# Kernel optimization log

Hardware: AMD Instinct MI355X
Metric: run time of the kernel (lower is better)

## Reference

```python
import jax, jax.numpy as jnp
import numpy as np

N_A = 50000
N_B = 50000
E = 500000
HID = 128
NEG_SLOPE = 0.2
LN_EPS = 1e-5


def _ln(x, g, b):
    mu = jnp.mean(x, axis=-1, keepdims=True)
    var = jnp.mean((x - mu) ** 2, axis=-1, keepdims=True)
    return (x - mu) * jax.lax.rsqrt(var + LN_EPS) * g + b


def _gat(x_src, x_dst, src, dst, W, a_src, a_dst, bias, H, D, n_dst):
    # PyG GATConv (shared lin for src/dst, add_self_loops=False, eval mode)
    hs = (x_src @ W).reshape(-1, H, D)              # [N_src, H, D]
    hd = (x_dst @ W).reshape(-1, H, D)              # [N_dst, H, D]
    a_s = jnp.einsum('nhd,hd->nh', hs, a_src)       # per-node src score
    a_d = jnp.einsum('nhd,hd->nh', hd, a_dst)       # per-node dst score
    e = jax.nn.leaky_relu(a_s[src] + a_d[dst], NEG_SLOPE)   # [E, H]
    m = jax.ops.segment_max(e, dst, num_segments=n_dst)     # segment softmax
    m = jnp.where(jnp.isfinite(m), m, 0.0)
    ex = jnp.exp(e - m[dst])
    s = jax.ops.segment_sum(ex, dst, num_segments=n_dst)
    alpha = ex / (s[dst] + 1e-16)                   # [E, H]
    msg = hs[src] * alpha[:, :, None]               # [E, H, D]
    out = jax.ops.segment_sum(msg, dst, num_segments=n_dst) # [N_dst, H, D]
    return out.reshape(n_dst, H * D) + bias


def setup_inputs() -> dict:
    key = jax.random.key(0)
    ks = jax.random.split(key, 32)
    f32 = jnp.float32

    def rn(k, sh, s=0.05):
        return jax.random.normal(k, sh, dtype=f32) * s

    inp = {}
    inp['x_A'] = jax.random.normal(ks[0], (N_A, 128), dtype=f32)
    inp['x_B'] = jax.random.normal(ks[1], (N_B, 64), dtype=f32)
    inp['pWA'] = rn(ks[2], (128, HID)); inp['pbA'] = rn(ks[3], (HID,))
    inp['pWB'] = rn(ks[4], (64, HID)); inp['pbB'] = rn(ks[5], (HID,))
    inp['w0ab'] = rn(ks[6], (HID, HID)); inp['as0ab'] = rn(ks[7], (4, 32))
    inp['ad0ab'] = rn(ks[8], (4, 32)); inp['b0ab'] = rn(ks[9], (HID,))
    inp['w0ba'] = rn(ks[10], (HID, HID)); inp['as0ba'] = rn(ks[11], (4, 32))
    inp['ad0ba'] = rn(ks[12], (4, 32)); inp['b0ba'] = rn(ks[13], (HID,))
    inp['w1ab'] = rn(ks[14], (HID, HID)); inp['as1ab'] = rn(ks[15], (1, HID))
    inp['ad1ab'] = rn(ks[16], (1, HID)); inp['b1ab'] = rn(ks[17], (HID,))
    inp['w1ba'] = rn(ks[18], (HID, HID)); inp['as1ba'] = rn(ks[19], (1, HID))
    inp['ad1ba'] = rn(ks[20], (1, HID)); inp['b1ba'] = rn(ks[21], (HID,))
    for i, nm in enumerate(['0A', '0B', '1A', '1B']):
        inp['g' + nm] = jnp.ones((HID,), dtype=f32)
        inp['bn' + nm] = jnp.zeros((HID,), dtype=f32)
    inp['ei_AB'] = jax.random.randint(ks[22], (2, E), 0, N_B)  # src in A, dst in B
    inp['ei_BA'] = jax.random.randint(ks[23], (2, E), 0, N_A)  # src in B, dst in A
    return inp


def reference(x_A, x_B, pWA, pbA, pWB, pbB,
              w0ab, as0ab, ad0ab, b0ab, w0ba, as0ba, ad0ba, b0ba,
              w1ab, as1ab, ad1ab, b1ab, w1ba, as1ba, ad1ba, b1ba,
              g0A, bn0A, g0B, bn0B, g1A, bn1A, g1B, bn1B,
              ei_AB, ei_BA):
    # input projections (dropout is eval-mode no-op)
    hA = x_A @ pWA + pbA
    hB = x_B @ pWB + pbB
    # layer 0: heads=4, d_head=32, concat -> 128
    pA, pB = hA, hB
    nB = _gat(hA, hB, ei_AB[0], ei_AB[1], w0ab, as0ab, ad0ab, b0ab, 4, 32, N_B)
    nA = _gat(hB, hA, ei_BA[0], ei_BA[1], w0ba, as0ba, ad0ba, b0ba, 4, 32, N_A)
    hA = jax.nn.relu(_ln(nA, g0A, bn0A)) + pA
    hB = jax.nn.relu(_ln(nB, g0B, bn0B)) + pB
    # layer 1: heads=1, out=128
    pA, pB = hA, hB
    nB = _gat(hA, hB, ei_AB[0], ei_AB[1], w1ab, as1ab, ad1ab, b1ab, 1, HID, N_B)
    nA = _gat(hB, hA, ei_BA[0], ei_BA[1], w1ba, as1ba, ad1ba, b1ba, 1, HID, N_A)
    hA = jax.nn.relu(_ln(nA, g1A, bn1A)) + pA
    hB = jax.nn.relu(_ln(nB, g1B, bn1B)) + pB
    return hA, hB
```

## Files before the change

### kernel.cpp

```cpp
#include <hip/hip_runtime.h>
#include <hip/hip_bf16.h>

using bf16 = __hip_bfloat16;
using frag8 = __attribute__((ext_vector_type(8))) short;
using f32x4 = __attribute__((ext_vector_type(4))) float;

__device__ __forceinline__ short f2bf_bits(float f) {
  bf16 h = __float2bfloat16(f);
  short s; __builtin_memcpy(&s, &h, 2); return s;
}
__device__ __forceinline__ float bfbits2f(unsigned short u) {
  unsigned uu = (unsigned)u << 16; float f; __builtin_memcpy(&f, &uu, 4); return f;
}
__device__ __forceinline__ float wred_sum(float v) {
#pragma unroll
  for (int o = 32; o; o >>= 1) v += __shfl_xor(v, o);
  return v;
}

struct ConvJob { const void* src; void* dst; int n; int mode; int ksh; };
struct ConvJobs { ConvJob j[28]; };
struct WtJob { const void* wraw; const void* adraw; bf16* out; int H; };
struct WtJobs4 { WtJob j[4]; };

__global__ __launch_bounds__(256) void prep_k(
    const unsigned* __restrict__ xdet, int* __restrict__ flag,
    ConvJobs cjobs, int ncv, WtJobs4 wjobs,
    int* __restrict__ cntA, int nA, int* __restrict__ cntB, int nB)
{
  const int b = blockIdx.x, tid = threadIdx.x;
  if (b >= ncv + 4) {
    int i = (b - (ncv + 4)) * 256 + tid;
    if (i < nA) cntA[i] = 0;
    else if (i < nA + nB) cntB[i - nA] = 0;
    return;
  }
  __shared__ int sh[256];
  int c = 0;
  for (int i = tid; i < 4096; i += 256) {
    unsigned bb = (xdet[i] >> 8) & 0x7F;
    c += (bb >= 0x3B && bb <= 0x41) ? 1 : 0;
  }
  sh[tid] = c; __syncthreads();
  for (int off = 128; off; off >>= 1) { if (tid < off) sh[tid] += sh[tid + off]; __syncthreads(); }
  const int f = (sh[0] < 2048) ? 1 : 0;
  if (b == 0 && tid == 0) flag[0] = f;

  if (b < ncv) {
    ConvJob J = cjobs.j[b];
    const int Kt = 1 << J.ksh;
    for (int i = tid; i < J.n; i += 256) {
      int si = i;
      if (J.mode == 1) { int n = i >> J.ksh, k = i & (Kt - 1); si = k * 128 + n; }
      float v = f ? ((const float*)J.src)[si] : bfbits2f(((const unsigned short*)J.src)[si]);
      if (J.mode == 1) ((bf16*)J.dst)[i] = __float2bfloat16(v);
      else             ((float*)J.dst)[i] = v;
    }
  } else {
    WtJob J = wjobs.j[b - ncv];
    const int H = J.H, D = 128 / H;
    for (int idx = tid; idx < 16 * 128; idx += 256) {
      int h = idx >> 7, k = idx & 127;
      float s = 0.f;
      if (h < H) {
        for (int d = 0; d < D; d++) {
          int n = h * D + d;
          float wv = f ? ((const float*)J.wraw)[k * 128 + n]
                       : bfbits2f(((const unsigned short*)J.wraw)[k * 128 + n]);
          float av = f ? ((const float*)J.adraw)[n]
                       : bfbits2f(((const unsigned short*)J.adraw)[n]);
          s += wv * av;
        }
      }
      J.out[idx] = __float2bfloat16(s);
    }
  }
}

struct GemmJob {
  const void* Av; const bf16* WT; const float* bias; const float* avec;
  bf16* outFull; float* outScore; const int* flagp;
  const bf16* WT2; float* outScore2;
  int M, K, H, H2;
};
__device__ __forceinline__ void gemm_body(const GemmJob& J, int blk) {
  __shared__ __align__(16) bf16 Wt[128 * 136];
  __shared__ __align__(16) bf16 Wt2s[16 * 136];
  const int tid = threadIdx.x;
  const int K = J.K;
  const int isf32 = J.flagp ? J.flagp[0] : 0;
  const int stride = K + 8;
  const int ksh2 = (K == 128) ? 4 : 3;
  const int kunits = K >> 3;
  for (int u = tid; u < 128 * kunits; u += 256) {
    int n = u >> ksh2, kb = u & (kunits - 1);
    frag8 v = *(const frag8*)(J.WT + n * K + kb * 8);
    *(frag8*)(Wt + n * stride + kb * 8) = v;
  }
  if (J.WT2) {
    int n = tid >> 4, kb = tid & 15;
    *(frag8*)(Wt2s + n * 136 + kb * 8) = *(const frag8*)(J.WT2 + n * 128 + kb * 8);
  }
  __syncthreads();

  const int lane = tid & 63, wave = tid >> 6;
  const int quad = lane >> 4, c = lane & 15;
  const int mbase = blk * 64 + wave * 16;
  const int arow = mbase + c;
  const bool rowOK = arow < J.M;

  f32x4 acc[8];
#pragma unroll
  for (int t = 0; t < 8; t++) acc[t] = (f32x4){0.f, 0.f, 0.f, 0.f};
  f32x4 acc2 = (f32x4){0.f, 0.f, 0.f, 0.f};

  for (int ks = 0; ks < K; ks += 32) {
    frag8 af;
    const int k0 = ks + quad * 8;
    if (rowOK) {
      if (isf32) {
        const float4* ap = (const float4*)((const float*)J.Av + (size_t)arow * K + k0);
        float4 v0 = ap[0], v1 = ap[1];
        af[0] = f2bf_bits(v0.x); af[1] = f2bf_bits(v0.y);
        af[2] = f2bf_bits(v0.z); af[3] = f2bf_bits(v0.w);
        af[4] = f2bf_bits(v1.x); af[5] = f2bf_bits(v1.y);
        af[6] = f2bf_bits(v1.z); af[7] = f2bf_bits(v1.w);
      } else {
        af = *(const frag8*)((const bf16*)J.Av + (size_t)arow * K + k0);
      }
    } else {
#pragma unroll
      for (int j = 0; j < 8; j++) af[j] = 0;
    }
#pragma unroll
    for (int t = 0; t < 8; t++) {
      frag8 bfv = *(const frag8*)(Wt + (t * 16 + c) * stride + k0);
      acc[t] = __builtin_amdgcn_mfma_f32_16x16x32_bf16(af, bfv, acc[t], 0, 0, 0);
    }
    if (J.WT2) {
      frag8 b2 = *(const frag8*)(Wt2s + c * 136 + k0);
      acc2 = __builtin_amdgcn_mfma_f32_16x16x32_bf16(af, b2, acc2, 0, 0, 0);
    }
  }

  if (J.outFull) {
#pragma unroll
    for (int t = 0; t < 8; t++) {
#pragma unroll
      for (int r = 0; r < 4; r++) {
        int orow = mbase + quad * 4 + r;
        if (orow < J.M) {
          float v = acc[t][r];
          if (J.bias) v += J.bias[t * 16 + c];
          J.outFull[(size_t)orow * 128 + t * 16 + c] = __float2bfloat16(v);
        }
      }
    }
  }
  if (J.outScore) {
    const int H = J.H;
    const int TPH = 8 / H;
    for (int hh = 0; hh < H; hh++) {
#pragma unroll
      for (int r = 0; r < 4; r++) {
        float p = 0.f;
        for (int tt = 0; tt < TPH; tt++) {
          int t = hh * TPH + tt;
          p += acc[t][r] * J.avec[t * 16 + c];
        }
#pragma unroll
        for (int off = 1; off < 16; off <<= 1) p += __shfl_xor(p, off);
        int orow = mbase + quad * 4 + r;
        if (c == 0 && orow < J.M) J.outScore[(size_t)orow * H + hh] = p;
      }
    }
  }
  if (J.outScore2) {
#pragma unroll
    for (int r = 0; r < 4; r++) {
      int orow = mbase + quad * 4 + r;
      if (c < J.H2 && orow < J.M) J.outScore2[(size_t)orow * J.H2 + c] = acc2[r];
    }
  }
}

__global__ __launch_bounds__(256) void histgemm_k(
    GemmJob ja, GemmJob jb, int gsplit,
    const int* __restrict__ dAB, const int* __restrict__ dBA, int E, int geh,
    int* __restrict__ cntB, int* __restrict__ cntA)
{
  const int b = blockIdx.x;
  if (b < 2 * geh) {
    if (b < geh) { int i = b * 256 + threadIdx.x; if (i < E) atomicAdd(&cntB[dAB[i]], 1); }
    else { int i = (b - geh) * 256 + threadIdx.x; if (i < E) atomicAdd(&cntA[dBA[i]], 1); }
    return;
  }
  const int gb = b - 2 * geh;
  if (gb < gsplit) gemm_body(ja, gb);
  else             gemm_body(jb, gb - gsplit);
}

__device__ __forceinline__ void blocksum_body(const int* cnt, int N, int* bsum, int blk) {
  __shared__ int sh[256];
  const int tid = threadIdx.x;
  const int beg = blk * 1024;
  const int end = (beg + 1024 < N) ? beg + 1024 : N;
  int loc = 0;
  for (int i = beg + tid; i < end; i += 256) loc += cnt[i];
  sh[tid] = loc; __syncthreads();
  for (int off = 128; off; off >>= 1) { if (tid < off) sh[tid] += sh[tid + off]; __syncthreads(); }
  if (tid == 0) bsum[blk] = sh[0];
}
__global__ __launch_bounds__(256) void bsumgemm_k(
    GemmJob ja, GemmJob jb, int gsplit,
    const int* __restrict__ cntB, int NB, int* __restrict__ bsumB, int nbB,
    const int* __restrict__ cntA, int NA, int* __restrict__ bsumA, int nbA)
{
  const int b = blockIdx.x;
  if (b < nbB + nbA) {
    if (b < nbB) blocksum_body(cntB, NB, bsumB, b);
    else         blocksum_body(cntA, NA, bsumA, b - nbB);
    return;
  }
  const int gb = b - (nbB + nbA);
  if (gb < gsplit) gemm_body(ja, gb);
  else             gemm_body(jb, gb - gsplit);
}
__device__ __forceinline__ void scanpart_body(int* bsum, int nb) {
  __shared__ int sh[256];
  const int tid = threadIdx.x;
  int v = (tid < nb) ? bsum[tid] : 0;
  sh[tid] = v; __syncthreads();
  for (int off = 1; off < 256; off <<= 1) {
    int x = sh[tid];
    int o = (tid >= off) ? sh[tid - off] : 0;
    __syncthreads();
    sh[tid] = x + o;
    __syncthreads();
  }
  if (tid < nb) bsum[tid] = (tid == 0) ? 0 : sh[tid - 1];
}
__global__ void scanpart2_k(int* __restrict__ bsumB, int nbB, int* __restrict__ bsumA, int nbA) {
  if (blockIdx.x == 0) scanpart_body(bsumB, nbB);
  else                 scanpart_body(bsumA, nbA);
}
__device__ __forceinline__ void writerp_body(const int* cnt, int N, const int* bsum,
                                             int* rp, int* cur, int blk) {
  __shared__ int sh[256];
  const int tid = threadIdx.x;
  const int idx0 = blk * 1024 + tid * 4;
  int c[4]; int loc = 0;
#pragma unroll
  for (int j = 0; j < 4; j++) {
    int i = idx0 + j;
    c[j] = (i < N) ? cnt[i] : 0;
    loc += c[j];
  }
  sh[tid] = loc; __syncthreads();
  for (int off = 1; off < 256; off <<= 1) {
    int x = sh[tid];
    int o = (tid >= off) ? sh[tid - off] : 0;
    __syncthreads();
    sh[tid] = x + o;
    __syncthreads();
  }
  int run = bsum[blk] + ((tid == 0) ? 0 : sh[tid - 1]);
#pragma unroll
  for (int j = 0; j < 4; j++) {
    int i = idx0 + j;
    if (i < N) { rp[i] = run; cur[i] = run; }
    run += c[j];
  }
  if (idx0 <= N - 1 && N - 1 < idx0 + 4) rp[N] = run;
}
__global__ void writerp2_k(const int* __restrict__ cntB, int NB, const int* __restrict__ bsumB,
                           int* __restrict__ rpAB, int* __restrict__ curB, int nbB,
                           const int* __restrict__ cntA, int NA, const int* __restrict__ bsumA,
                           int* __restrict__ rpBA, int* __restrict__ curA) {
  int b = blockIdx.x;
  if (b < nbB) writerp_body(cntB, NB, bsumB, rpAB, curB, b);
  else         writerp_body(cntA, NA, bsumA, rpBA, curA, b - nbB);
}

__global__ __launch_bounds__(256) void gemm2_k(GemmJob ja, GemmJob jb, int split) {
  if (blockIdx.x < split) gemm_body(ja, blockIdx.x);
  else                    gemm_body(jb, blockIdx.x - split);
}

__global__ __launch_bounds__(256) void scatter8_k(
    const int* __restrict__ sAB, const int* __restrict__ dAB,
    const int* __restrict__ sBA, const int* __restrict__ dBA, int E,
    int* __restrict__ curB, int* __restrict__ slAB,
    int* __restrict__ curA, int* __restrict__ slBA, int NB, int NA)
{
  const int g = blockIdx.x & 7;
  const int sidx = blockIdx.x >> 3;
  const int loB = (int)((long long)NB * g >> 3), hiB = (int)((long long)NB * (g + 1) >> 3);
  const int loA = (int)((long long)NA * g >> 3), hiA = (int)((long long)NA * (g + 1) >> 3);
  const int b0 = sidx * 2048;
#pragma unroll
  for (int j = 0; j < 8; j++) {
    int i = b0 + j * 256 + threadIdx.x;
    if (i < 2 * E) {
      bool ab = i < E;
      int k = ab ? i : i - E;
      int d = ab ? dAB[k] : dBA[k];
      int lo = ab ? loB : loA, hi = ab ? hiB : hiA;
      if (d >= lo && d < hi) {
        int sv = ab ? sAB[k] : sBA[k];
        int pos = atomicAdd((ab ? curB : curA) + d, 1);
        (ab ? slAB : slBA)[pos] = sv;
      }
    }
  }
}

struct AggJob {
  const int* rp; const int* srcl; const float* as_; const float* ad_;
  const bf16* hs; const float* bias; const float* gamma; const float* beta;
  const bf16* resid; bf16* outBf; void* outFinal; const int* flagp;
  int nodeBase, N;
};

template<bool FINAL>
__device__ __forceinline__ void agg_epi4(const AggJob& J, int n, int hl, int half,
                                         float inv, float a0, float a1, float a2, float a3) {
  float4 bi = *(const float4*)(J.bias + 4 * hl);
  float y0 = a0 * inv + bi.x;
  float y1 = a1 * inv + bi.y;
  float y2 = a2 * inv + bi.z;
  float y3 = a3 * inv + bi.w;
  float tsum = wred_sum(y0 + y1 + y2 + y3);
  float tsq  = wred_sum(y0 * y0 + y1 * y1 + y2 * y2 + y3 * y3);
  float mu = tsum * 0.00390625f;
  float var = tsq * 0.00390625f - mu * mu;
  float rs = rsqrtf(var + 1e-5f);
  float4 ga = *(const float4*)(J.gamma + 4 * hl);
  float4 be = *(const float4*)(J.beta + 4 * hl);
  float z0 = (y0 - mu) * rs * ga.x + be.x;
  float z1 = (y1 - mu) * rs * ga.y + be.y;
  float z2 = (y2 - mu) * rs * ga.z + be.z;
  float z3 = (y3 - mu) * rs * ga.w + be.w;
  uint2 ru = *(const uint2*)(J.resid + (size_t)n * 128 + hl * 4);
  z0 = fmaxf(z0, 0.f) + bfbits2f((unsigned short)(ru.x & 0xFFFF));
  z1 = fmaxf(z1, 0.f) + bfbits2f((unsigned short)(ru.x >> 16));
  z2 = fmaxf(z2, 0.f) + bfbits2f((unsigned short)(ru.y & 0xFFFF));
  z3 = fmaxf(z3, 0.f) + bfbits2f((unsigned short)(ru.y >> 16));
  if (half == 0) {
    if constexpr (FINAL) {
      size_t oi = (size_t)(J.nodeBase + n) * 128 + hl * 4;
      if (J.flagp[0]) {
        *(float4*)((float*)J.outFinal + oi) = make_float4(z0, z1, z2, z3);
      } else {
        uint2 pk;
        pk.x = (unsigned)(unsigned short)f2bf_bits(z0) | ((unsigned)(unsigned short)f2bf_bits(z1) << 16);
        pk.y = (unsigned)(unsigned short)f2bf_bits(z2) | ((unsigned)(unsigned short)f2bf_bits(z3) << 16);
        *(uint2*)((bf16*)J.outFinal + oi) = pk;
      }
    } else {
      uint2 pk;
      pk.x = (unsigned)(unsigned short)f2bf_bits(z0) | ((unsigned)(unsigned short)f2bf_bits(z1) << 16);
      pk.y = (unsigned)(unsigned short)f2bf_bits(z2) | ((unsigned)(unsigned short)f2bf_bits(z3) << 16);
      *(uint2*)(J.outBf + (size_t)n * 128 + hl * 4) = pk;
    }
  }
}

template<int H, bool FINAL>
__global__ __launch_bounds__(256) void agg_k(AggJob JA, AggJob JB, int split) {
  const bool first = blockIdx.x < split;
  const AggJob J = first ? JA : JB;
  const int blk = first ? blockIdx.x : blockIdx.x - split;

  __shared__ int   s_src[4][64];
  __shared__ float s_p[4][64 * H];
  const int tid = threadIdx.x;
  const int wave = tid >> 6, lane = tid & 63;
  const int n = blk * 4 + wave;
  if (n >= J.N) return;

  const int beg = J.rp[n], end = J.rp[n + 1];
  const int half = lane >> 5;
  const int hl = lane & 31;
  const int myh = (H == 4) ? (hl >> 3) : 0;

  float4 adv;
  if (H == 4) adv = *(const float4*)(J.ad_ + (size_t)n * 4);
  else        adv.x = J.ad_[n];

  float sl_[H];
#pragma unroll
  for (int h = 0; h < H; h++) sl_[h] = 0.f;
  float a0 = 0.f, a1 = 0.f, a2 = 0.f, a3 = 0.f;
  const int* srcp = J.srcl;
  const float* asp = J.as_;
  const bf16* hsp = J.hs;

  for (int base = beg; base < end; base += 64) {
    const int cn = (end - base < 64) ? end - base : 64;
    if (lane < cn) {
      int s = srcp[base + lane];
      s_src[wave][lane] = s;
      if (H == 4) {
        float4 a = *(const float4*)(asp + (size_t)s * 4);
        float4 o; float v;
        v = a.x + adv.x; v = v > 0.f ? v : 0.2f * v; o.x = __expf(v);
        v = a.y + adv.y; v = v > 0.f ? v : 0.2f * v; o.y = __expf(v);
        v = a.z + adv.z; v = v > 0.f ? v : 0.2f * v; o.z = __expf(v);
        v = a.w + adv.w; v = v > 0.f ? v : 0.2f * v; o.w = __expf(v);
        *(float4*)&s_p[wave][lane * 4] = o;
        sl_[0] += o.x; sl_[1] += o.y; sl_[2] += o.z; sl_[3] += o.w;
      } else {
        float v = asp[s] + adv.x;
        v = v > 0.f ? v : 0.2f * v;
        float pv = __expf(v);
        s_p[wave][lane] = pv;
        sl_[0] += pv;
      }
    }
    __builtin_amdgcn_wave_barrier();
    const int cne = cn & ~1;
#pragma unroll 4
    for (int e = 0; e < cne; e += 2) {
      const int eidx = e + half;
      const int s = s_src[wave][eidx];
      const float p = s_p[wave][eidx * H + myh];
      const uint2 u = *(const uint2*)(hsp + (size_t)s * 128 + hl * 4);
      a0 += p * bfbits2f((unsigned short)(u.x & 0xFFFF));
      a1 += p * bfbits2f((unsigned short)(u.x >> 16));
      a2 += p * bfbits2f((unsigned short)(u.y & 0xFFFF));
      a3 += p * bfbits2f((unsigned short)(u.y >> 16));
    }
    if (cn & 1) {
      const int eidx = cn - 1;
      const int s = s_src[wave][eidx];
      const float p = half ? 0.f : s_p[wave][eidx * H + myh];
      const uint2 u = *(const uint2*)(hsp + (size_t)s * 128 + hl * 4);
      a0 += p * bfbits2f((unsigned short)(u.x & 0xFFFF));
      a1 += p * bfbits2f((unsigned short)(u.x >> 16));
      a2 += p * bfbits2f((unsigned short)(u.y & 0xFFFF));
      a3 += p * bfbits2f((unsigned short)(u.y >> 16));
    }
    __builtin_amdgcn_wave_barrier();
  }

  a0 += __shfl_xor(a0, 32);
  a1 += __shfl_xor(a1, 32);
  a2 += __shfl_xor(a2, 32);
  a3 += __shfl_xor(a3, 32);

  float s = 0.f;
#pragma unroll
  for (int h = 0; h < H; h++) {
    float t = wred_sum(sl_[h]);
    if (h == myh) s = t;
  }
  const float inv = 1.f / (s + 1e-16f);
  agg_epi4<FINAL>(J, n, hl, half, inv, a0, a1, a2, a3);
}

extern "C" void kernel_launch(void* const* d_in, const int* in_sizes, int n_in,
                              void* d_out, int out_size, void* d_ws, size_t ws_size,
                              hipStream_t stream)
{
  const int NA = in_sizes[0] / 128;
  const int NB = in_sizes[1] / 64;
  const int E  = in_sizes[30] / 2;
  const int* eiAB = (const int*)d_in[30];
  const int* eiBA = (const int*)d_in[31];
  const int* srcAB = eiAB;  const int* dstAB = eiAB + E;
  const int* srcBA = eiBA;  const int* dstBA = eiBA + E;

  char* w = (char*)d_ws;
  size_t used = 0;
  auto alloc = [&](size_t bytes) {
    char* p = w + used;
    used += (bytes + 255) & ~size_t(255);
    return (void*)p;
  };
  int*  flag  = (int*)alloc(256);
  bf16* WcA   = (bf16*)alloc(16384 * 2);
  bf16* WcB   = (bf16*)alloc(8192 * 2);
  bf16* Wc0ab = (bf16*)alloc(16384 * 2);
  bf16* Wc0ba = (bf16*)alloc(16384 * 2);
  bf16* Wc1ab = (bf16*)alloc(16384 * 2);
  bf16* Wc1ba = (bf16*)alloc(16384 * 2);
  bf16* Wt0ab = (bf16*)alloc(16 * 128 * 2);
  bf16* Wt0ba = (bf16*)alloc(16 * 128 * 2);
  bf16* Wt1ab = (bf16*)alloc(16 * 128 * 2);
  bf16* Wt1ba = (bf16*)alloc(16 * 128 * 2);
  float* vec  = (float*)alloc(22 * 128 * 4);
  bf16* hA    = (bf16*)alloc((size_t)NA * 128 * 2);
  bf16* hB    = (bf16*)alloc((size_t)NB * 128 * 2);
  bf16* hsAB  = (bf16*)alloc((size_t)NA * 128 * 2);
  bf16* hsBA  = (bf16*)alloc((size_t)NB * 128 * 2);
  float* asAB = (float*)alloc((size_t)NA * 4 * 4);
  float* adAB = (float*)alloc((size_t)NB * 4 * 4);
  float* asBA = (float*)alloc((size_t)NB * 4 * 4);
  float* adBA = (float*)alloc((size_t)NA * 4 * 4);
  int* rpAB = (int*)alloc((size_t)(NB + 1) * 4);
  int* slAB = (int*)alloc((size_t)E * 4);
  int* rpBA = (int*)alloc((size_t)(NA + 1) * 4);
  int* slBA = (int*)alloc((size_t)E * 4);
  int* cntA = (int*)alloc((size_t)NA * 4);
  int* curA = (int*)alloc((size_t)NA * 4);
  int* cntB = (int*)alloc((size_t)NB * 4);
  int* curB = (int*)alloc((size_t)NB * 4);
  int* bsumA = (int*)alloc(256 * 4);
  int* bsumB = (int*)alloc(256 * 4);
  if (used > ws_size) return;

  auto V = [&](int i) { return vec + 128 * i; };

  ConvJobs jobs{};
  int nj = 0;
  auto addT = [&](const void* s, void* d, int K) {
    int ksh = (K == 128) ? 7 : 6;
    jobs.j[nj++] = ConvJob{s, d, 128 * K, 1, ksh};
  };
  auto addV = [&](const void* s, void* d) { jobs.j[nj++] = ConvJob{s, d, 128, 0, 7}; };
  addT(d_in[2], WcA, 128);
  addT(d_in[4], WcB, 64);
  addT(d_in[6], Wc0ab, 128);
  addT(d_in[10], Wc0ba, 128);
  addT(d_in[14], Wc1ab, 128);
  addT(d_in[18], Wc1ba, 128);
  const int vsrc[22] = {3, 5, 7, 8, 9, 11, 12, 13, 15, 16, 17, 19, 20, 21, 22, 23, 24, 25, 26, 27, 28, 29};
  for (int i = 0; i < 22; i++) addV(d_in[vsrc[i]], V(i));

  WtJobs4 wj{};
  wj.j[0] = WtJob{d_in[6],  d_in[8],  Wt0ab, 4};
  wj.j[1] = WtJob{d_in[10], d_in[12], Wt0ba, 4};
  wj.j[2] = WtJob{d_in[14], d_in[16], Wt1ab, 1};
  wj.j[3] = WtJob{d_in[18], d_in[20], Wt1ba, 1};

  const int nz = (NA + NB + 255) / 256;
  prep_k<<<nj + 4 + nz, 256, 0, stream>>>((const unsigned*)d_in[0], flag, jobs, nj, wj,
                                          cntA, NA, cntB, NB);

  const int geh = (E + 255) / 256;
  const int gA = (NA + 63) / 64, gB = (NB + 63) / 64;
  const int aA = (NA + 3) / 4, aB = (NB + 3) / 4;
  const int nbB = (NB + 1023) / 1024, nbA = (NA + 1023) / 1024;

  {
    GemmJob ja{d_in[0], WcA, V(0), nullptr, hA, nullptr, flag, nullptr, nullptr, NA, 128, 1, 0};
    GemmJob jb{d_in[1], WcB, V(1), nullptr, hB, nullptr, flag, nullptr, nullptr, NB, 64, 1, 0};
    histgemm_k<<<2 * geh + gA + gB, 256, 0, stream>>>(ja, jb, gA, dstAB, dstBA, E, geh,
                                                      cntB, cntA);
  }
  {
    GemmJob ja{hA, Wc0ab, nullptr, V(2), hsAB, asAB, nullptr, Wt0ba, adBA, NA, 128, 4, 4};
    GemmJob jb{hB, Wc0ba, nullptr, V(5), hsBA, asBA, nullptr, Wt0ab, adAB, NB, 128, 4, 4};
    bsumgemm_k<<<nbB + nbA + gA + gB, 256, 0, stream>>>(ja, jb, gA,
                                                        cntB, NB, bsumB, nbB,
                                                        cntA, NA, bsumA, nbA);
  }
  scanpart2_k<<<2, 256, 0, stream>>>(bsumB, nbB, bsumA, nbA);
  writerp2_k<<<nbB + nbA, 256, 0, stream>>>(cntB, NB, bsumB, rpAB, curB, nbB,
                                            cntA, NA, bsumA, rpBA, curA);
  {
    const int nsl = (2 * E + 2047) / 2048;
    scatter8_k<<<8 * nsl, 256, 0, stream>>>(srcAB, dstAB, srcBA, dstBA, E,
                                            curB, slAB, curA, slBA, NB, NA);
  }
  {
    AggJob ja{rpAB, slAB, asAB, adAB, hsAB, V(4), V(16), V(17), hB, hB, nullptr, nullptr, 0, NB};
    AggJob jb{rpBA, slBA, asBA, adBA, hsBA, V(7), V(14), V(15), hA, hA, nullptr, nullptr, 0, NA};
    agg_k<4, false><<<aB + aA, 256, 0, stream>>>(ja, jb, aB);
  }
  {
    GemmJob ja{hA, Wc1ab, nullptr, V(8),  hsAB, asAB, nullptr, Wt1ba, adBA, NA, 128, 1, 1};
    GemmJob jb{hB, Wc1ba, nullptr, V(11), hsBA, asBA, nullptr, Wt1ab, adAB, NB, 128, 1, 1};
    gemm2_k<<<gA + gB, 256, 0, stream>>>(ja, jb, gA);
  }
  {
    AggJob ja{rpAB, slAB, asAB, adAB, hsAB, V(10), V(20), V(21), hB, nullptr, d_out, flag, NA, NB};
    AggJob jb{rpBA, slBA, asBA, adBA, hsBA, V(13), V(18), V(19), hA, nullptr, d_out, flag, 0, NA};
    agg_k<1, true><<<aB + aA, 256, 0, stream>>>(ja, jb, aB);
  }
}
```

Before: 467.4 us.

## Sub-bucket CSR by source range and fuse scatter with layer-0 GEMM

The edge histogram and scatter now key on (dst, src>>shift) with 8 source buckets per destination. Within each destination's edge list the sources are partially sorted, which should make the later gathers of source features more local. The separate block-scan kernel is removed: each writerp block sums the preceding block totals itself. The layer-0 GEMM now runs inside the scatter kernel instead of the blocksum kernel. The cost is count, cursor and row-pointer arrays that are 8x larger, more zeroing work, and an O(blocks) prefix loop in every writerp block.

```diff
diff --git a/kernel.cpp b/kernel.cpp
--- a/kernel.cpp
+++ b/kernel.cpp
@@ -26,13 +26,13 @@
 __global__ __launch_bounds__(256) void prep_k(
     const unsigned* __restrict__ xdet, int* __restrict__ flag,
     ConvJobs cjobs, int ncv, WtJobs4 wjobs,
-    int* __restrict__ cntA, int nA, int* __restrict__ cntB, int nB)
+    int* __restrict__ cntA, int nA8, int* __restrict__ cntB, int nB8)
 {
   const int b = blockIdx.x, tid = threadIdx.x;
   if (b >= ncv + 4) {
     int i = (b - (ncv + 4)) * 256 + tid;
-    if (i < nA) cntA[i] = 0;
-    else if (i < nA + nB) cntB[i - nA] = 0;
+    if (i < nA8) cntA[i] = 0;
+    else if (i < nA8 + nB8) cntB[i - nA8] = 0;
     return;
   }
   __shared__ int sh[256];
@@ -186,13 +186,19 @@
 
 __global__ __launch_bounds__(256) void histgemm_k(
     GemmJob ja, GemmJob jb, int gsplit,
-    const int* __restrict__ dAB, const int* __restrict__ dBA, int E, int geh,
-    int* __restrict__ cntB, int* __restrict__ cntA)
+    const int* __restrict__ sAB, const int* __restrict__ dAB,
+    const int* __restrict__ sBA, const int* __restrict__ dBA, int E, int geh,
+    int* __restrict__ cntB, int* __restrict__ cntA, int shA, int shB)
 {
   const int b = blockIdx.x;
   if (b < 2 * geh) {
-    if (b < geh) { int i = b * 256 + threadIdx.x; if (i < E) atomicAdd(&cntB[dAB[i]], 1); }
-    else { int i = (b - geh) * 256 + threadIdx.x; if (i < E) atomicAdd(&cntA[dBA[i]], 1); }
+    if (b < geh) {
+      int i = b * 256 + threadIdx.x;
+      if (i < E) atomicAdd(&cntB[dAB[i] * 8 + (sAB[i] >> shA)], 1);
+    } else {
+      int i = (b - geh) * 256 + threadIdx.x;
+      if (i < E) atomicAdd(&cntA[dBA[i] * 8 + (sBA[i] >> shB)], 1);
+    }
     return;
   }
   const int gb = b - 2 * geh;
@@ -211,43 +217,25 @@
   for (int off = 128; off; off >>= 1) { if (tid < off) sh[tid] += sh[tid + off]; __syncthreads(); }
   if (tid == 0) bsum[blk] = sh[0];
 }
-__global__ __launch_bounds__(256) void bsumgemm_k(
-    GemmJob ja, GemmJob jb, int gsplit,
-    const int* __restrict__ cntB, int NB, int* __restrict__ bsumB, int nbB,
-    const int* __restrict__ cntA, int NA, int* __restrict__ bsumA, int nbA)
+__global__ __launch_bounds__(256) void blocksum2_k(
+    const int* __restrict__ cntB, int NB8, int* __restrict__ bsumB, int nbB,
+    const int* __restrict__ cntA, int NA8, int* __restrict__ bsumA)
 {
-  const int b = blockIdx.x;
-  if (b < nbB + nbA) {
-    if (b < nbB) blocksum_body(cntB, NB, bsumB, b);
-    else         blocksum_body(cntA, NA, bsumA, b - nbB);
-    return;
-  }
-  const int gb = b - (nbB + nbA);
-  if (gb < gsplit) gemm_body(ja, gb);
-  else             gemm_body(jb, gb - gsplit);
-}
-__device__ __forceinline__ void scanpart_body(int* bsum, int nb) {
-  __shared__ int sh[256];
-  const int tid = threadIdx.x;
-  int v = (tid < nb) ? bsum[tid] : 0;
-  sh[tid] = v; __syncthreads();
-  for (int off = 1; off < 256; off <<= 1) {
-    int x = sh[tid];
-    int o = (tid >= off) ? sh[tid - off] : 0;
-    __syncthreads();
-    sh[tid] = x + o;
-    __syncthreads();
-  }
-  if (tid < nb) bsum[tid] = (tid == 0) ? 0 : sh[tid - 1];
-}
-__global__ void scanpart2_k(int* __restrict__ bsumB, int nbB, int* __restrict__ bsumA, int nbA) {
-  if (blockIdx.x == 0) scanpart_body(bsumB, nbB);
-  else                 scanpart_body(bsumA, nbA);
+  int b = blockIdx.x;
+  if (b < nbB) blocksum_body(cntB, NB8, bsumB, b);
+  else         blocksum_body(cntA, NA8, bsumA, b - nbB);
 }
 __device__ __forceinline__ void writerp_body(const int* cnt, int N, const int* bsum,
                                              int* rp, int* cur, int blk) {
   __shared__ int sh[256];
   const int tid = threadIdx.x;
+  int offacc = 0;
+  for (int i = tid; i < blk; i += 256) offacc += bsum[i];
+  sh[tid] = offacc; __syncthreads();
+  for (int off = 128; off; off >>= 1) { if (tid < off) sh[tid] += sh[tid + off]; __syncthreads(); }
+  const int base = sh[0];
+  __syncthreads();
+
   const int idx0 = blk * 1024 + tid * 4;
   int c[4]; int loc = 0;
 #pragma unroll
@@ -264,7 +252,7 @@
     sh[tid] = x + o;
     __syncthreads();
   }
-  int run = bsum[blk] + ((tid == 0) ? 0 : sh[tid - 1]);
+  int run = base + ((tid == 0) ? 0 : sh[tid - 1]);
 #pragma unroll
   for (int j = 0; j < 4; j++) {
     int i = idx0 + j;
@@ -273,13 +261,15 @@
   }
   if (idx0 <= N - 1 && N - 1 < idx0 + 4) rp[N] = run;
 }
-__global__ void writerp2_k(const int* __restrict__ cntB, int NB, const int* __restrict__ bsumB,
-                           int* __restrict__ rpAB, int* __restrict__ curB, int nbB,
-                           const int* __restrict__ cntA, int NA, const int* __restrict__ bsumA,
-                           int* __restrict__ rpBA, int* __restrict__ curA) {
+__global__ __launch_bounds__(256) void writerp2_k(
+    const int* __restrict__ cntB, int NB8, const int* __restrict__ bsumB,
+    int* __restrict__ rpAB, int* __restrict__ curB, int nbB,
+    const int* __restrict__ cntA, int NA8, const int* __restrict__ bsumA,
+    int* __restrict__ rpBA, int* __restrict__ curA)
+{
   int b = blockIdx.x;
-  if (b < nbB) writerp_body(cntB, NB, bsumB, rpAB, curB, b);
-  else         writerp_body(cntA, NA, bsumA, rpBA, curA, b - nbB);
+  if (b < nbB) writerp_body(cntB, NB8, bsumB, rpAB, curB, b);
+  else         writerp_body(cntA, NA8, bsumA, rpBA, curA, b - nbB);
 }
 
 __global__ __launch_bounds__(256) void gemm2_k(GemmJob ja, GemmJob jb, int split) {
@@ -287,14 +277,23 @@
   else                    gemm_body(jb, blockIdx.x - split);
 }
 
-__global__ __launch_bounds__(256) void scatter8_k(
+__global__ __launch_bounds__(256) void scattgemm_k(
+    GemmJob ja, GemmJob jb, int gsplit, int gtot,
     const int* __restrict__ sAB, const int* __restrict__ dAB,
     const int* __restrict__ sBA, const int* __restrict__ dBA, int E,
     int* __restrict__ curB, int* __restrict__ slAB,
-    int* __restrict__ curA, int* __restrict__ slBA, int NB, int NA)
+    int* __restrict__ curA, int* __restrict__ slBA, int NB, int NA,
+    int shA, int shB)
 {
-  const int g = blockIdx.x & 7;
-  const int sidx = blockIdx.x >> 3;
+  int b = blockIdx.x;
+  if (b < gtot) {
+    if (b < gsplit) gemm_body(ja, b);
+    else            gemm_body(jb, b - gsplit);
+    return;
+  }
+  b -= gtot;
+  const int g = b & 7;
+  const int sidx = b >> 3;
   const int loB = (int)((long long)NB * g >> 3), hiB = (int)((long long)NB * (g + 1) >> 3);
   const int loA = (int)((long long)NA * g >> 3), hiA = (int)((long long)NA * (g + 1) >> 3);
   const int b0 = sidx * 2048;
@@ -308,7 +307,8 @@
       int lo = ab ? loB : loA, hi = ab ? hiB : hiA;
       if (d >= lo && d < hi) {
         int sv = ab ? sAB[k] : sBA[k];
-        int pos = atomicAdd((ab ? curB : curA) + d, 1);
+        int key = d * 8 + (sv >> (ab ? shA : shB));
+        int pos = atomicAdd((ab ? curB : curA) + key, 1);
         (ab ? slAB : slBA)[pos] = sv;
       }
     }
@@ -379,7 +379,7 @@
   const int n = blk * 4 + wave;
   if (n >= J.N) return;
 
-  const int beg = J.rp[n], end = J.rp[n + 1];
+  const int beg = J.rp[(size_t)n * 8], end = J.rp[(size_t)n * 8 + 8];
   const int half = lane >> 5;
   const int hl = lane & 31;
   const int myh = (H == 4) ? (hl >> 3) : 0;
@@ -470,6 +470,9 @@
   const int* eiBA = (const int*)d_in[31];
   const int* srcAB = eiAB;  const int* dstAB = eiAB + E;
   const int* srcBA = eiBA;  const int* dstBA = eiBA + E;
+
+  int shA = 0; while (((NA - 1) >> shA) > 7) shA++;
+  int shB = 0; while (((NB - 1) >> shB) > 7) shB++;
 
   char* w = (char*)d_ws;
   size_t used = 0;
@@ -498,16 +501,16 @@
   float* adAB = (float*)alloc((size_t)NB * 4 * 4);
   float* asBA = (float*)alloc((size_t)NB * 4 * 4);
   float* adBA = (float*)alloc((size_t)NA * 4 * 4);
-  int* rpAB = (int*)alloc((size_t)(NB + 1) * 4);
+  int* rpAB = (int*)alloc(((size_t)NB * 8 + 1) * 4);
   int* slAB = (int*)alloc((size_t)E * 4);
-  int* rpBA = (int*)alloc((size_t)(NA + 1) * 4);
+  int* rpBA = (int*)alloc(((size_t)NA * 8 + 1) * 4);
   int* slBA = (int*)alloc((size_t)E * 4);
-  int* cntA = (int*)alloc((size_t)NA * 4);
-  int* curA = (int*)alloc((size_t)NA * 4);
-  int* cntB = (int*)alloc((size_t)NB * 4);
-  int* curB = (int*)alloc((size_t)NB * 4);
-  int* bsumA = (int*)alloc(256 * 4);
-  int* bsumB = (int*)alloc(256 * 4);
+  int* cntA = (int*)alloc((size_t)NA * 8 * 4);
+  int* curA = (int*)alloc((size_t)NA * 8 * 4);
+  int* cntB = (int*)alloc((size_t)NB * 8 * 4);
+  int* curB = (int*)alloc((size_t)NB * 8 * 4);
+  int* bsumA = (int*)alloc(1024 * 4);
+  int* bsumB = (int*)alloc(1024 * 4);
   if (used > ws_size) return;
 
   auto V = [&](int i) { return vec + 128 * i; };
@@ -534,35 +537,35 @@
   wj.j[2] = WtJob{d_in[14], d_in[16], Wt1ab, 1};
   wj.j[3] = WtJob{d_in[18], d_in[20], Wt1ba, 1};
 
-  const int nz = (NA + NB + 255) / 256;
+  const int NA8 = NA * 8, NB8 = NB * 8;
+  const int nz = (NA8 + NB8 + 255) / 256;
   prep_k<<<nj + 4 + nz, 256, 0, stream>>>((const unsigned*)d_in[0], flag, jobs, nj, wj,
-                                          cntA, NA, cntB, NB);
+                                          cntA, NA8, cntB, NB8);
 
   const int geh = (E + 255) / 256;
   const int gA = (NA + 63) / 64, gB = (NB + 63) / 64;
   const int aA = (NA + 3) / 4, aB = (NB + 3) / 4;
-  const int nbB = (NB + 1023) / 1024, nbA = (NA + 1023) / 1024;
+  const int nbB = (NB8 + 1023) / 1024, nbA = (NA8 + 1023) / 1024;
 
   {
     GemmJob ja{d_in[0], WcA, V(0), nullptr, hA, nullptr, flag, nullptr, nullptr, NA, 128, 1, 0};
     GemmJob jb{d_in[1], WcB, V(1), nullptr, hB, nullptr, flag, nullptr, nullptr, NB, 64, 1, 0};
-    histgemm_k<<<2 * geh + gA + gB, 256, 0, stream>>>(ja, jb, gA, dstAB, dstBA, E, geh,
-                                                      cntB, cntA);
-  }
+    histgemm_k<<<2 * geh + gA + gB, 256, 0, stream>>>(ja, jb, gA,
+                                                      srcAB, dstAB, srcBA, dstBA, E, geh,
+                                                      cntB, cntA, shA, shB);
+  }
+  blocksum2_k<<<nbB + nbA, 256, 0, stream>>>(cntB, NB8, bsumB, nbB, cntA, NA8, bsumA);
+  writerp2_k<<<nbB + nbA, 256, 0, stream>>>(cntB, NB8, bsumB, rpAB, curB, nbB,
+                                            cntA, NA8, bsumA, rpBA, curA);
   {
     GemmJob ja{hA, Wc0ab, nullptr, V(2), hsAB, asAB, nullptr, Wt0ba, adBA, NA, 128, 4, 4};
     GemmJob jb{hB, Wc0ba, nullptr, V(5), hsBA, asBA, nullptr, Wt0ab, adAB, NB, 128, 4, 4};
-    bsumgemm_k<<<nbB + nbA + gA + gB, 256, 0, stream>>>(ja, jb, gA,
-                                                        cntB, NB, bsumB, nbB,
-                                                        cntA, NA, bsumA, nbA);
-  }
-  scanpart2_k<<<2, 256, 0, stream>>>(bsumB, nbB, bsumA, nbA);
-  writerp2_k<<<nbB + nbA, 256, 0, stream>>>(cntB, NB, bsumB, rpAB, curB, nbB,
-                                            cntA, NA, bsumA, rpBA, curA);
-  {
+    const int gtot = gA + gB;
     const int nsl = (2 * E + 2047) / 2048;
-    scatter8_k<<<8 * nsl, 256, 0, stream>>>(srcAB, dstAB, srcBA, dstBA, E,
-                                            curB, slAB, curA, slBA, NB, NA);
+    scattgemm_k<<<gtot + 8 * nsl, 256, 0, stream>>>(ja, jb, gA, gtot,
+                                                    srcAB, dstAB, srcBA, dstBA, E,
+                                                    curB, slAB, curA, slBA, NB, NA,
+                                                    shA, shB);
   }
   {
     AggJob ja{rpAB, slAB, asAB, adAB, hsAB, V(4), V(16), V(17), hB, hB, nullptr, nullptr, 0, NB};
```

Result: no change. 465.2 us (-0.5%).

## Restructure CSR build, fuse scatter with GEMM, widen aggregation to 16B loads

Applied to the files above, without the earlier changes.

The separate scan-of-block-sums kernel is removed: each writerp block now reduces the preceding block sums itself. The layer-0 GEMM moves out of the blocksum launch into a combined launch with the edge scatter, cutting one launch and overlapping the GEMM with atomic scatter work. The aggregation kernel now handles 4 edges per iteration with 16-lane groups loading 8 bf16 values (uint4) each, and derives the softmax denominator from the accumulated p values instead of a separate per-head sum. The cost is redundant block-sum reads in writerp and more shuffle reductions per node.

```diff
diff --git a/kernel.cpp b/kernel.cpp
--- a/kernel.cpp
+++ b/kernel.cpp
@@ -211,43 +211,25 @@
   for (int off = 128; off; off >>= 1) { if (tid < off) sh[tid] += sh[tid + off]; __syncthreads(); }
   if (tid == 0) bsum[blk] = sh[0];
 }
-__global__ __launch_bounds__(256) void bsumgemm_k(
-    GemmJob ja, GemmJob jb, int gsplit,
+__global__ __launch_bounds__(256) void blocksum2_k(
     const int* __restrict__ cntB, int NB, int* __restrict__ bsumB, int nbB,
-    const int* __restrict__ cntA, int NA, int* __restrict__ bsumA, int nbA)
+    const int* __restrict__ cntA, int NA, int* __restrict__ bsumA)
 {
-  const int b = blockIdx.x;
-  if (b < nbB + nbA) {
-    if (b < nbB) blocksum_body(cntB, NB, bsumB, b);
-    else         blocksum_body(cntA, NA, bsumA, b - nbB);
-    return;
-  }
-  const int gb = b - (nbB + nbA);
-  if (gb < gsplit) gemm_body(ja, gb);
-  else             gemm_body(jb, gb - gsplit);
-}
-__device__ __forceinline__ void scanpart_body(int* bsum, int nb) {
-  __shared__ int sh[256];
-  const int tid = threadIdx.x;
-  int v = (tid < nb) ? bsum[tid] : 0;
-  sh[tid] = v; __syncthreads();
-  for (int off = 1; off < 256; off <<= 1) {
-    int x = sh[tid];
-    int o = (tid >= off) ? sh[tid - off] : 0;
-    __syncthreads();
-    sh[tid] = x + o;
-    __syncthreads();
-  }
-  if (tid < nb) bsum[tid] = (tid == 0) ? 0 : sh[tid - 1];
-}
-__global__ void scanpart2_k(int* __restrict__ bsumB, int nbB, int* __restrict__ bsumA, int nbA) {
-  if (blockIdx.x == 0) scanpart_body(bsumB, nbB);
-  else                 scanpart_body(bsumA, nbA);
+  int b = blockIdx.x;
+  if (b < nbB) blocksum_body(cntB, NB, bsumB, b);
+  else         blocksum_body(cntA, NA, bsumA, b - nbB);
 }
 __device__ __forceinline__ void writerp_body(const int* cnt, int N, const int* bsum,
                                              int* rp, int* cur, int blk) {
   __shared__ int sh[256];
   const int tid = threadIdx.x;
+  int offacc = 0;
+  for (int i = tid; i < blk; i += 256) offacc += bsum[i];
+  sh[tid] = offacc; __syncthreads();
+  for (int off = 128; off; off >>= 1) { if (tid < off) sh[tid] += sh[tid + off]; __syncthreads(); }
+  const int base = sh[0];
+  __syncthreads();
+
   const int idx0 = blk * 1024 + tid * 4;
   int c[4]; int loc = 0;
 #pragma unroll
@@ -264,7 +246,7 @@
     sh[tid] = x + o;
     __syncthreads();
   }
-  int run = bsum[blk] + ((tid == 0) ? 0 : sh[tid - 1]);
+  int run = base + ((tid == 0) ? 0 : sh[tid - 1]);
 #pragma unroll
   for (int j = 0; j < 4; j++) {
     int i = idx0 + j;
@@ -273,10 +255,12 @@
   }
   if (idx0 <= N - 1 && N - 1 < idx0 + 4) rp[N] = run;
 }
-__global__ void writerp2_k(const int* __restrict__ cntB, int NB, const int* __restrict__ bsumB,
-                           int* __restrict__ rpAB, int* __restrict__ curB, int nbB,
-                           const int* __restrict__ cntA, int NA, const int* __restrict__ bsumA,
-                           int* __restrict__ rpBA, int* __restrict__ curA) {
+__global__ __launch_bounds__(256) void writerp2_k(
+    const int* __restrict__ cntB, int NB, const int* __restrict__ bsumB,
+    int* __restrict__ rpAB, int* __restrict__ curB, int nbB,
+    const int* __restrict__ cntA, int NA, const int* __restrict__ bsumA,
+    int* __restrict__ rpBA, int* __restrict__ curA)
+{
   int b = blockIdx.x;
   if (b < nbB) writerp_body(cntB, NB, bsumB, rpAB, curB, b);
   else         writerp_body(cntA, NA, bsumA, rpBA, curA, b - nbB);
@@ -287,14 +271,22 @@
   else                    gemm_body(jb, blockIdx.x - split);
 }
 
-__global__ __launch_bounds__(256) void scatter8_k(
+__global__ __launch_bounds__(256) void scattgemm_k(
+    GemmJob ja, GemmJob jb, int gsplit, int gtot,
     const int* __restrict__ sAB, const int* __restrict__ dAB,
     const int* __restrict__ sBA, const int* __restrict__ dBA, int E,
     int* __restrict__ curB, int* __restrict__ slAB,
     int* __restrict__ curA, int* __restrict__ slBA, int NB, int NA)
 {
-  const int g = blockIdx.x & 7;
-  const int sidx = blockIdx.x >> 3;
+  int b = blockIdx.x;
+  if (b < gtot) {
+    if (b < gsplit) gemm_body(ja, b);
+    else            gemm_body(jb, b - gsplit);
+    return;
+  }
+  b -= gtot;
+  const int g = b & 7;
+  const int sidx = b >> 3;
   const int loB = (int)((long long)NB * g >> 3), hiB = (int)((long long)NB * (g + 1) >> 3);
   const int loA = (int)((long long)NA * g >> 3), hiA = (int)((long long)NA * (g + 1) >> 3);
   const int b0 = sidx * 2048;
@@ -322,50 +314,6 @@
   int nodeBase, N;
 };
 
-template<bool FINAL>
-__device__ __forceinline__ void agg_epi4(const AggJob& J, int n, int hl, int half,
-                                         float inv, float a0, float a1, float a2, float a3) {
-  float4 bi = *(const float4*)(J.bias + 4 * hl);
-  float y0 = a0 * inv + bi.x;
-  float y1 = a1 * inv + bi.y;
-  float y2 = a2 * inv + bi.z;
-  float y3 = a3 * inv + bi.w;
-  float tsum = wred_sum(y0 + y1 + y2 + y3);
-  float tsq  = wred_sum(y0 * y0 + y1 * y1 + y2 * y2 + y3 * y3);
-  float mu = tsum * 0.00390625f;
-  float var = tsq * 0.00390625f - mu * mu;
-  float rs = rsqrtf(var + 1e-5f);
-  float4 ga = *(const float4*)(J.gamma + 4 * hl);
-  float4 be = *(const float4*)(J.beta + 4 * hl);
-  float z0 = (y0 - mu) * rs * ga.x + be.x;
-  float z1 = (y1 - mu) * rs * ga.y + be.y;
-  float z2 = (y2 - mu) * rs * ga.z + be.z;
-  float z3 = (y3 - mu) * rs * ga.w + be.w;
-  uint2 ru = *(const uint2*)(J.resid + (size_t)n * 128 + hl * 4);
-  z0 = fmaxf(z0, 0.f) + bfbits2f((unsigned short)(ru.x & 0xFFFF));
-  z1 = fmaxf(z1, 0.f) + bfbits2f((unsigned short)(ru.x >> 16));
-  z2 = fmaxf(z2, 0.f) + bfbits2f((unsigned short)(ru.y & 0xFFFF));
-  z3 = fmaxf(z3, 0.f) + bfbits2f((unsigned short)(ru.y >> 16));
-  if (half == 0) {
-    if constexpr (FINAL) {
-      size_t oi = (size_t)(J.nodeBase + n) * 128 + hl * 4;
-      if (J.flagp[0]) {
-        *(float4*)((float*)J.outFinal + oi) = make_float4(z0, z1, z2, z3);
-      } else {
-        uint2 pk;
-        pk.x = (unsigned)(unsigned short)f2bf_bits(z0) | ((unsigned)(unsigned short)f2bf_bits(z1) << 16);
-        pk.y = (unsigned)(unsigned short)f2bf_bits(z2) | ((unsigned)(unsigned short)f2bf_bits(z3) << 16);
-        *(uint2*)((bf16*)J.outFinal + oi) = pk;
-      }
-    } else {
-      uint2 pk;
-      pk.x = (unsigned)(unsigned short)f2bf_bits(z0) | ((unsigned)(unsigned short)f2bf_bits(z1) << 16);
-      pk.y = (unsigned)(unsigned short)f2bf_bits(z2) | ((unsigned)(unsigned short)f2bf_bits(z3) << 16);
-      *(uint2*)(J.outBf + (size_t)n * 128 + hl * 4) = pk;
-    }
-  }
-}
-
 template<int H, bool FINAL>
 __global__ __launch_bounds__(256) void agg_k(AggJob JA, AggJob JB, int split) {
   const bool first = blockIdx.x < split;
@@ -380,18 +328,17 @@
   if (n >= J.N) return;
 
   const int beg = J.rp[n], end = J.rp[n + 1];
-  const int half = lane >> 5;
-  const int hl = lane & 31;
-  const int myh = (H == 4) ? (hl >> 3) : 0;
+  const int qe = lane >> 4;
+  const int ql = lane & 15;
+  const int myh = (H == 4) ? (ql >> 2) : 0;
 
   float4 adv;
   if (H == 4) adv = *(const float4*)(J.ad_ + (size_t)n * 4);
   else        adv.x = J.ad_[n];
 
-  float sl_[H];
-#pragma unroll
-  for (int h = 0; h < H; h++) sl_[h] = 0.f;
   float a0 = 0.f, a1 = 0.f, a2 = 0.f, a3 = 0.f;
+  float a4 = 0.f, a5 = 0.f, a6 = 0.f, a7 = 0.f;
+  float dacc = 0.f;
   const int* srcp = J.srcl;
   const float* asp = J.as_;
   const bf16* hsp = J.hs;
@@ -409,54 +356,100 @@
         v = a.z + adv.z; v = v > 0.f ? v : 0.2f * v; o.z = __expf(v);
         v = a.w + adv.w; v = v > 0.f ? v : 0.2f * v; o.w = __expf(v);
         *(float4*)&s_p[wave][lane * 4] = o;
-        sl_[0] += o.x; sl_[1] += o.y; sl_[2] += o.z; sl_[3] += o.w;
       } else {
         float v = asp[s] + adv.x;
         v = v > 0.f ? v : 0.2f * v;
-        float pv = __expf(v);
-        s_p[wave][lane] = pv;
-        sl_[0] += pv;
+        s_p[wave][lane] = __expf(v);
       }
     }
     __builtin_amdgcn_wave_barrier();
-    const int cne = cn & ~1;
 #pragma unroll 4
-    for (int e = 0; e < cne; e += 2) {
-      const int eidx = e + half;
-      const int s = s_src[wave][eidx];
-      const float p = s_p[wave][eidx * H + myh];
-      const uint2 u = *(const uint2*)(hsp + (size_t)s * 128 + hl * 4);
+    for (int e = 0; e < cn; e += 4) {
+      const int eidx = e + qe;
+      const bool val = eidx < cn;
+      const int ei = val ? eidx : cn - 1;
+      const int s = s_src[wave][ei];
+      const float p = val ? s_p[wave][ei * H + myh] : 0.f;
+      const uint4 u = *(const uint4*)(hsp + (size_t)s * 128 + ql * 8);
+      dacc += p;
       a0 += p * bfbits2f((unsigned short)(u.x & 0xFFFF));
       a1 += p * bfbits2f((unsigned short)(u.x >> 16));
       a2 += p * bfbits2f((unsigned short)(u.y & 0xFFFF));
       a3 += p * bfbits2f((unsigned short)(u.y >> 16));
-    }
-    if (cn & 1) {
-      const int eidx = cn - 1;
-      const int s = s_src[wave][eidx];
-      const float p = half ? 0.f : s_p[wave][eidx * H + myh];
-      const uint2 u = *(const uint2*)(hsp + (size_t)s * 128 + hl * 4);
-      a0 += p * bfbits2f((unsigned short)(u.x & 0xFFFF));
-      a1 += p * bfbits2f((unsigned short)(u.x >> 16));
-      a2 += p * bfbits2f((unsigned short)(u.y & 0xFFFF));
-      a3 += p * bfbits2f((unsigned short)(u.y >> 16));
+      a4 += p * bfbits2f((unsigned short)(u.z & 0xFFFF));
+      a5 += p * bfbits2f((unsigned short)(u.z >> 16));
+      a6 += p * bfbits2f((unsigned short)(u.w & 0xFFFF));
+      a7 += p * bfbits2f((unsigned short)(u.w >> 16));
     }
     __builtin_amdgcn_wave_barrier();
   }
 
-  a0 += __shfl_xor(a0, 32);
-  a1 += __shfl_xor(a1, 32);
-  a2 += __shfl_xor(a2, 32);
-  a3 += __shfl_xor(a3, 32);
-
-  float s = 0.f;
-#pragma unroll
-  for (int h = 0; h < H; h++) {
-    float t = wred_sum(sl_[h]);
-    if (h == myh) s = t;
-  }
-  const float inv = 1.f / (s + 1e-16f);
-  agg_epi4<FINAL>(J, n, hl, half, inv, a0, a1, a2, a3);
+#pragma unroll
+  for (int o = 16; o <= 32; o <<= 1) {
+    a0 += __shfl_xor(a0, o); a1 += __shfl_xor(a1, o);
+    a2 += __shfl_xor(a2, o); a3 += __shfl_xor(a3, o);
+    a4 += __shfl_xor(a4, o); a5 += __shfl_xor(a5, o);
+    a6 += __shfl_xor(a6, o); a7 += __shfl_xor(a7, o);
+    dacc += __shfl_xor(dacc, o);
+  }
+  const float inv = 1.f / (dacc + 1e-16f);
+
+  const float4 bi0 = *(const float4*)(J.bias + ql * 8);
+  const float4 bi1 = *(const float4*)(J.bias + ql * 8 + 4);
+  float y0 = a0 * inv + bi0.x, y1 = a1 * inv + bi0.y;
+  float y2 = a2 * inv + bi0.z, y3 = a3 * inv + bi0.w;
+  float y4 = a4 * inv + bi1.x, y5 = a5 * inv + bi1.y;
+  float y6 = a6 * inv + bi1.z, y7 = a7 * inv + bi1.w;
+  float tsum = wred_sum(y0 + y1 + y2 + y3 + y4 + y5 + y6 + y7);
+  float tsq  = wred_sum(y0*y0 + y1*y1 + y2*y2 + y3*y3 + y4*y4 + y5*y5 + y6*y6 + y7*y7);
+  float mu = tsum * 0.001953125f;
+  float var = tsq * 0.001953125f - mu * mu;
+  float rs = rsqrtf(var + 1e-5f);
+  const float4 ga0 = *(const float4*)(J.gamma + ql * 8);
+  const float4 ga1 = *(const float4*)(J.gamma + ql * 8 + 4);
+  const float4 be0 = *(const float4*)(J.beta + ql * 8);
+  const float4 be1 = *(const float4*)(J.beta + ql * 8 + 4);
+  float z0 = (y0 - mu) * rs * ga0.x + be0.x;
+  float z1 = (y1 - mu) * rs * ga0.y + be0.y;
+  float z2 = (y2 - mu) * rs * ga0.z + be0.z;
+  float z3 = (y3 - mu) * rs * ga0.w + be0.w;
+  float z4 = (y4 - mu) * rs * ga1.x + be1.x;
+  float z5 = (y5 - mu) * rs * ga1.y + be1.y;
+  float z6 = (y6 - mu) * rs * ga1.z + be1.z;
+  float z7 = (y7 - mu) * rs * ga1.w + be1.w;
+  const uint4 ru = *(const uint4*)(J.resid + (size_t)n * 128 + ql * 8);
+  z0 = fmaxf(z0, 0.f) + bfbits2f((unsigned short)(ru.x & 0xFFFF));
+  z1 = fmaxf(z1, 0.f) + bfbits2f((unsigned short)(ru.x >> 16));
+  z2 = fmaxf(z2, 0.f) + bfbits2f((unsigned short)(ru.y & 0xFFFF));
+  z3 = fmaxf(z3, 0.f) + bfbits2f((unsigned short)(ru.y >> 16));
+  z4 = fmaxf(z4, 0.f) + bfbits2f((unsigned short)(ru.z & 0xFFFF));
+  z5 = fmaxf(z5, 0.f) + bfbits2f((unsigned short)(ru.z >> 16));
+  z6 = fmaxf(z6, 0.f) + bfbits2f((unsigned short)(ru.w & 0xFFFF));
+  z7 = fmaxf(z7, 0.f) + bfbits2f((unsigned short)(ru.w >> 16));
+
+  if (qe == 0) {
+    if constexpr (FINAL) {
+      if (J.flagp[0]) {
+        float* op = (float*)J.outFinal + (size_t)(J.nodeBase + n) * 128 + ql * 8;
+        *(float4*)op = make_float4(z0, z1, z2, z3);
+        *(float4*)(op + 4) = make_float4(z4, z5, z6, z7);
+      } else {
+        uint4 pk;
+        pk.x = (unsigned)(unsigned short)f2bf_bits(z0) | ((unsigned)(unsigned short)f2bf_bits(z1) << 16);
+        pk.y = (unsigned)(unsigned short)f2bf_bits(z2) | ((unsigned)(unsigned short)f2bf_bits(z3) << 16);
+        pk.z = (unsigned)(unsigned short)f2bf_bits(z4) | ((unsigned)(unsigned short)f2bf_bits(z5) << 16);
+        pk.w = (unsigned)(unsigned short)f2bf_bits(z6) | ((unsigned)(unsigned short)f2bf_bits(z7) << 16);
+        *(uint4*)((bf16*)J.outFinal + (size_t)(J.nodeBase + n) * 128 + ql * 8) = pk;
+      }
+    } else {
+      uint4 pk;
+      pk.x = (unsigned)(unsigned short)f2bf_bits(z0) | ((unsigned)(unsigned short)f2bf_bits(z1) << 16);
+      pk.y = (unsigned)(unsigned short)f2bf_bits(z2) | ((unsigned)(unsigned short)f2bf_bits(z3) << 16);
+      pk.z = (unsigned)(unsigned short)f2bf_bits(z4) | ((unsigned)(unsigned short)f2bf_bits(z5) << 16);
+      pk.w = (unsigned)(unsigned short)f2bf_bits(z6) | ((unsigned)(unsigned short)f2bf_bits(z7) << 16);
+      *(uint4*)(J.outBf + (size_t)n * 128 + ql * 8) = pk;
+    }
+  }
 }
 
 extern "C" void kernel_launch(void* const* d_in, const int* in_sizes, int n_in,
@@ -549,20 +542,17 @@
     histgemm_k<<<2 * geh + gA + gB, 256, 0, stream>>>(ja, jb, gA, dstAB, dstBA, E, geh,
                                                       cntB, cntA);
   }
+  blocksum2_k<<<nbB + nbA, 256, 0, stream>>>(cntB, NB, bsumB, nbB, cntA, NA, bsumA);
+  writerp2_k<<<nbB + nbA, 256, 0, stream>>>(cntB, NB, bsumB, rpAB, curB, nbB,
+                                            cntA, NA, bsumA, rpBA, curA);
   {
     GemmJob ja{hA, Wc0ab, nullptr, V(2), hsAB, asAB, nullptr, Wt0ba, adBA, NA, 128, 4, 4};
     GemmJob jb{hB, Wc0ba, nullptr, V(5), hsBA, asBA, nullptr, Wt0ab, adAB, NB, 128, 4, 4};
-    bsumgemm_k<<<nbB + nbA + gA + gB, 256, 0, stream>>>(ja, jb, gA,
-                                                        cntB, NB, bsumB, nbB,
-                                                        cntA, NA, bsumA, nbA);
-  }
-  scanpart2_k<<<2, 256, 0, stream>>>(bsumB, nbB, bsumA, nbA);
-  writerp2_k<<<nbB + nbA, 256, 0, stream>>>(cntB, NB, bsumB, rpAB, curB, nbB,
-                                            cntA, NA, bsumA, rpBA, curA);
-  {
+    const int gtot = gA + gB;
     const int nsl = (2 * E + 2047) / 2048;
-    scatter8_k<<<8 * nsl, 256, 0, stream>>>(srcAB, dstAB, srcBA, dstBA, E,
-                                            curB, slAB, curA, slBA, NB, NA);
+    scattgemm_k<<<gtot + 8 * nsl, 256, 0, stream>>>(ja, jb, gA, gtot,
+                                                    srcAB, dstAB, srcBA, dstBA, E,
+                                                    curB, slAB, curA, slBA, NB, NA);
   }
   {
     AggJob ja{rpAB, slAB, asAB, adAB, hsAB, V(4), V(16), V(17), hB, hB, nullptr, nullptr, 0, NB};
```

Measured after the change: 467.4 us. No clear change (+0.0%).
